# Optimization experiments

Measured on AMD Instinct MI355X. Metric: run time of the kernel, lower is better.

Reference implementation:

```python
import jax, jax.numpy as jnp
import numpy as np

E = 20000      # num edges
S = 64         # mul of 0e (scalar) channels
V = 32         # mul of 1o (vector) channels
FC_IN = 128    # radial basis length
HID = 64       # fc hidden width
INV_SQRT3 = 0.5773502691896258  # CG(1o x 1o -> 0e) = delta_ij / sqrt(3)


def setup_inputs() -> dict:
    key = jax.random.key(0)
    ks = jax.random.split(key, 16)
    n = jax.random.normal
    return {
        # edge features, layout [64 scalars | 32 vectors * 3 comps]
        "fea_in1": n(ks[0], (E, S + 3 * V), jnp.float32),
        "fea_in2": n(ks[1], (E, S + 3 * V), jnp.float32),
        "fea_weight": n(ks[2], (E, FC_IN), jnp.float32),
        # FullyConnectedTensorProduct internal weights (e3nn init: normal(0,1))
        "w_ss_s": n(ks[3], (S, S, S), jnp.float32),   # 0e x 0e -> 64x0e scalars
        "w_vv_s": n(ks[4], (V, V, S), jnp.float32),   # 1o x 1o -> 64x0e scalars
        "w_ss_g": n(ks[5], (S, S, V), jnp.float32),   # 0e x 0e -> 32x0e gates
        "w_vv_g": n(ks[6], (V, V, V), jnp.float32),   # 1o x 1o -> 32x0e gates
        "w_sv_v": n(ks[7], (S, V, V), jnp.float32),   # 0e x 1o -> 32x1o
        "w_vs_v": n(ks[8], (V, S, V), jnp.float32),   # 1o x 0e -> 32x1o
        # fc MLP: Linear(128,64) SiLU Linear(64,64) SiLU Linear(64,96)
        "fc_w1": n(ks[9], (FC_IN, HID), jnp.float32) / np.sqrt(FC_IN).astype(np.float32),
        "fc_b1": jnp.zeros((HID,), jnp.float32),
        "fc_w2": n(ks[10], (HID, HID), jnp.float32) / np.sqrt(HID).astype(np.float32),
        "fc_b2": jnp.zeros((HID,), jnp.float32),
        "fc_w3": n(ks[11], (HID, S + V), jnp.float32) / np.sqrt(HID).astype(np.float32),
        "fc_b3": jnp.zeros((S + V,), jnp.float32),
        "batch_edge": jnp.zeros((E,), jnp.int32),  # unused (norm='')
    }


def _equiconv(fea_in1, fea_in2, fea_weight,
              w_ss_s, w_vv_s, w_ss_g, w_vv_g, w_sv_v, w_vs_v,
              fc_w1, fc_b1, fc_w2, fc_b2, fc_w3, fc_b3):
    x1s, x1v = fea_in1[:, :S], fea_in1[:, S:].reshape(-1, V, 3)
    x2s, x2v = fea_in2[:, :S], fea_in2[:, S:].reshape(-1, V, 3)

    # path normalization: 1/sqrt(fan_in), fan_in = sum(mul1*mul2) over paths to output
    a_sc = 1.0 / np.sqrt(S * S + V * V).astype(np.float32)
    a_vec = 1.0 / np.sqrt(2 * S * V).astype(np.float32)

    # FullyConnectedTensorProduct (uvw connectivity)
    sc = a_sc * (jnp.einsum('eu,ev,uvw->ew', x1s, x2s, w_ss_s)
                 + INV_SQRT3 * jnp.einsum('eui,evi,uvw->ew', x1v, x2v, w_vv_s))
    g = a_sc * (jnp.einsum('eu,ev,uvw->ew', x1s, x2s, w_ss_g)
                + INV_SQRT3 * jnp.einsum('eui,evi,uvw->ew', x1v, x2v, w_vv_g))
    vec = a_vec * (jnp.einsum('eu,evi,uvw->ewi', x1s, x2v, w_sv_v)
                   + jnp.einsum('eui,ev,uvw->ewi', x1v, x2s, w_vs_v))

    # Gate: silu on scalars, sigmoid gates multiply the l>0 part
    sc = jax.nn.silu(sc)
    vec = vec * jax.nn.sigmoid(g)[:, :, None]

    # fc MLP producing per-channel elementwise conv weights
    h = jax.nn.silu(fea_weight @ fc_w1 + fc_b1)
    h = jax.nn.silu(h @ fc_w2 + fc_b2)
    w = h @ fc_w3 + fc_b3  # [E, S+V]

    # e3ElementWise: one scalar weight per channel (shared over m components)
    sc = sc * w[:, :S]
    vec = vec * w[:, S:, None]
    return jnp.concatenate([sc, vec.reshape(-1, 3 * V)], axis=-1)


def reference(fea_in1, fea_in2, fea_weight,
              w_ss_s, w_vv_s, w_ss_g, w_vv_g, w_sv_v, w_vs_v,
              fc_w1, fc_b1, fc_w2, fc_b2, fc_w3, fc_b3, batch_edge):
    del batch_edge  # only used by optional e3LayerNorm (norm='')
    return _equiconv(fea_in1, fea_in2, fea_weight,
                     w_ss_s, w_vv_s, w_ss_g, w_vv_g, w_sv_v, w_vs_v,
                     fc_w1, fc_b1, fc_w2, fc_b2, fc_w3, fc_b3)
```

## Files before the change

### kernel.cpp

```cpp
#include <hip/hip_runtime.h>


#define E_TOT 20000

typedef __attribute__((ext_vector_type(8))) short short8;
typedef __attribute__((ext_vector_type(4))) float f32x4;
typedef __attribute__((ext_vector_type(2))) __bf16 bf16x2;

#define FRAG_USH 512
#define HALF_USH 1536
#define CH_USH   3072
#define N_CH     52
#define NSLOT    5
#define STRIDE_W 159744
#define FC1_OFF  638976
#define FC2_OFF  647168
#define FC3_OFF  651264
#define WS_USH   657408

#define X1S_OFF  61440
#define X1V_OFF  65664
#define POOL_B   71936

__device__ __forceinline__ unsigned short f2b(float f){
  return __builtin_bit_cast(unsigned short, (__bf16)f);
}
__device__ __forceinline__ unsigned f2b2(float lo, float hi){
  bf16x2 t; t[0] = (__bf16)lo; t[1] = (__bf16)hi;
  return __builtin_bit_cast(unsigned, t);
}
__device__ __forceinline__ float b2f(unsigned short h){
  return __uint_as_float(((unsigned)h) << 16);
}
__device__ __forceinline__ f32x4 mfma16(short8 a, short8 b, f32x4 c){
  return __builtin_amdgcn_mfma_f32_16x16x32_bf16(a, b, c, 0, 0, 0);
}
union U8 { short8 v; unsigned u[4]; };
__device__ __forceinline__ float silu_f(float x){ return x/(1.f+__expf(-x)); }
__device__ __forceinline__ float sigm_f(float x){ return 1.f/(1.f+__expf(-x)); }

#define PACK8(a, s, x) \
  a.u[0]=f2b2((s)*(x)[0],(s)*(x)[1]); a.u[1]=f2b2((s)*(x)[2],(s)*(x)[3]); \
  a.u[2]=f2b2((s)*(x)[4],(s)*(x)[5]); a.u[3]=f2b2((s)*(x)[6],(s)*(x)[7]);

#define WV(code) { __builtin_amdgcn_s_waitcnt(code); __builtin_amdgcn_sched_barrier(0); }
#define WL3      { __builtin_amdgcn_s_waitcnt(0xC37F); __builtin_amdgcn_sched_barrier(0); }

__device__ __forceinline__ int fpos(int kl, int n16){
  return (kl>>3)*128 + n16*8 + (kl&7);
}

__global__ void prep_weights(const float* __restrict__ ss_s, const float* __restrict__ ss_g,
                             const float* __restrict__ vv_s, const float* __restrict__ vv_g,
                             const float* __restrict__ sv,   const float* __restrict__ vs,
                             const float* __restrict__ w1,   const float* __restrict__ w2,
                             const float* __restrict__ w3,   unsigned short* __restrict__ wsb)
{
  int g = blockIdx.x * 256 + threadIdx.x;
  if (g >= WS_USH/8) return;
  const int dest = g << 3;
  const float A_SC  = 0.013975424859373686f;
  const float A_VV  = (float)(0.013975424859373686 * 0.5773502691896258);
  const float A_VEC = 0.015625f;

  const float* src = nullptr;
  int stride = 0;
  float scale = 1.f;

  if (dest < FC1_OFF) {
    int wave = dest / STRIDE_W;
    int off  = dest - wave*STRIDE_W;
    int c    = off / CH_USH;
    int rem  = off - c*CH_USH;
    int t    = rem >> 9;
    int p    = rem & 511;
    int kl   = (p >> 7) << 3;
    int n16  = (p >> 3) & 15;
    if (c < 32) {
      int u = (wave<<4) + (c>>1);
      int v = ((c&1)<<5) + kl;
      if (t < 4) { src = ss_s + (u<<12)+(v<<6)+((t<<4)+n16);     stride = 64; }
      else       { src = ss_g + (u<<11)+(v<<5)+(((t-4)<<4)+n16); stride = 32; }
      scale = A_SC;
    } else if (c < 40) {
      int u = (wave<<3) + (c-32);
      int v = kl;
      if (t < 4) { src = vv_s + (u<<11)+(v<<6)+((t<<4)+n16);     stride = 64; }
      else       { src = vv_g + (u<<10)+(v<<5)+(((t-4)<<4)+n16); stride = 32; }
      scale = A_VV;
    } else if (c < 46) {
      int ul = (c-40)*3 + (t>>1);
      if (ul < 16) {
        int u = (wave<<4) + ul;
        src = sv + (u<<10)+(kl<<5)+(((t&1)<<4)+n16);
        stride = 32; scale = A_VEC;
      }
    } else {
      int cc = c - 46;
      int vh = cc/3, ch3 = cc - vh*3;
      int fseq = ch3*6 + t;
      if (fseq < 16) {
        int u = (wave<<3) + (fseq>>1);
        int v = (vh<<5) + kl;
        src = vs + (u<<11)+(v<<5)+(((fseq&1)<<4)+n16);
        stride = 32; scale = A_VEC;
      }
    }
  } else if (dest < FC2_OFF) {
    int off = dest - FC1_OFF;
    int fi = off >> 9, p = off & 511;
    int kl = (p>>7)<<3, n16 = (p>>3)&15;
    int k = ((fi>>2)<<5) + kl, n = ((fi&3)<<4) + n16;
    src = w1 + (k<<6) + n; stride = 64;
  } else if (dest < FC3_OFF) {
    int off = dest - FC2_OFF;
    int fi = off >> 9, p = off & 511;
    int kl = (p>>7)<<3, n16 = (p>>3)&15;
    int k = ((fi>>2)<<5) + kl, n = ((fi&3)<<4) + n16;
    src = w2 + (k<<6) + n; stride = 64;
  } else {
    int off = dest - FC3_OFF;
    int fi = off >> 9, p = off & 511;
    int kl = (p>>7)<<3, n16 = (p>>3)&15;
    int koff = fi/6, nhi = fi - koff*6;
    int k = (koff<<5) + kl, n = (nhi<<4) + n16;
    src = w3 + k*96 + n; stride = 96;
  }

  U8 a;
  if (src) {
    float v0 = scale * src[0*stride], v1 = scale * src[1*stride];
    float v2 = scale * src[2*stride], v3 = scale * src[3*stride];
    float v4 = scale * src[4*stride], v5 = scale * src[5*stride];
    float v6 = scale * src[6*stride], v7 = scale * src[7*stride];
    a.u[0] = f2b2(v0, v1); a.u[1] = f2b2(v2, v3);
    a.u[2] = f2b2(v4, v5); a.u[3] = f2b2(v6, v7);
  } else {
    a.u[0] = 0; a.u[1] = 0; a.u[2] = 0; a.u[3] = 0;
  }
  *(short8*)(wsb + dest) = a.v;
}

__global__ __launch_bounds__(256, 2)
void equiconv_main(const float* __restrict__ fea1,
                   const float* __restrict__ fea2,
                   const float* __restrict__ few,
                   const float* __restrict__ fb1,
                   const float* __restrict__ fb2,
                   const float* __restrict__ fb3,
                   const unsigned short* __restrict__ wsb,
                   float* __restrict__ out)
{
  __shared__ __align__(16) unsigned char pool[POOL_B];
  unsigned short* ring = (unsigned short*)pool;
  unsigned short* x1s_ = (unsigned short*)(pool + X1S_OFF);
  unsigned short* x1v_ = (unsigned short*)(pool + X1V_OFF);
  unsigned short* hb_  = (unsigned short*)(pool + X1S_OFF);
  float*          redf = (float*)pool;

  #define X1S(r, cc) x1s_[(r)*66 + (cc)]
  #define X1V(r, cc) x1v_[(r)*98 + (cc)]
  #define HB(w, r, cc) hb_[(((w)<<4) + (r))*72 + (cc)]

  const int tid  = threadIdx.x;
  const int lane = tid & 63, wv = tid >> 6;
  const int ln   = lane & 15, quad = lane >> 4, q8 = quad << 3;
  const int ebase = blockIdx.x << 5;

  for (int it = tid; it < 1280; it += 256){
    int row = it / 40, seg = it - row*40;
    float4 v1 = *(const float4*)(fea1 + (size_t)(ebase + row)*160 + seg*4);
    const float* p1 = (const float*)&v1;
    int c0 = seg*4;
    #pragma unroll
    for (int jj = 0; jj < 4; jj++){
      int col = c0 + jj;
      if (col < 64) X1S(row, col) = f2b(p1[jj]);
      else          X1V(row, col-64) = f2b(p1[jj]);
    }
  }
  __syncthreads();

  float xe[2][8], xo[2][8], y0[2][8], y1[2][8], y2[2][8];
  #pragma unroll
  for (int s = 0; s < 2; s++){
    const float* p = fea2 + (size_t)(ebase + s*16 + ln)*160;
    float4 a0 = *(const float4*)(p + q8);
    float4 a1 = *(const float4*)(p + q8 + 4);
    float4 b0 = *(const float4*)(p + 32 + q8);
    float4 b1 = *(const float4*)(p + 36 + q8);
    xe[s][0]=a0.x; xe[s][1]=a0.y; xe[s][2]=a0.z; xe[s][3]=a0.w;
    xe[s][4]=a1.x; xe[s][5]=a1.y; xe[s][6]=a1.z; xe[s][7]=a1.w;
    xo[s][0]=b0.x; xo[s][1]=b0.y; xo[s][2]=b0.z; xo[s][3]=b0.w;
    xo[s][4]=b1.x; xo[s][5]=b1.y; xo[s][6]=b1.z; xo[s][7]=b1.w;
    const float* py = p + 64 + q8*3;
    float yb[24];
    #pragma unroll
    for (int t = 0; t < 12; t++){
      float2 f2v = *(const float2*)(py + 2*t);
      yb[2*t] = f2v.x; yb[2*t+1] = f2v.y;
    }
    #pragma unroll
    for (int j = 0; j < 8; j++){
      y0[s][j] = yb[3*j]; y1[s][j] = yb[3*j+1]; y2[s][j] = yb[3*j+2];
    }
  }

  const unsigned short* gstream = wsb + (size_t)wv*STRIDE_W;
  const int rbase = wv*NSLOT*HALF_USH;
  auto issue_half = [&](int h){
    const unsigned short* g = gstream + h*HALF_USH + lane*8;
    unsigned short* l = &ring[rbase + (h%NSLOT)*HALF_USH];
    #pragma unroll
    for (int q = 0; q < 3; q++)
      __builtin_amdgcn_global_load_lds(
        (const __attribute__((address_space(1))) unsigned int*)(g + q*FRAG_USH),
        (__attribute__((address_space(3))) unsigned int*)(l + q*FRAG_USH),
        16, 0, 0);
  };
  issue_half(0); issue_half(1); issue_half(2); issue_half(3);

  const int r0 = ln, r1 = 16 + ln;
  const f32x4 z4 = {0.f,0.f,0.f,0.f};
  f32x4 accS[2][6] = {{z4,z4,z4,z4,z4,z4},{z4,z4,z4,z4,z4,z4}};
  f32x4 accV[2][3][2] = {{{z4,z4},{z4,z4},{z4,z4}},{{z4,z4},{z4,z4},{z4,z4}}};

  #define READCH(cc, bb, WAC, WBC, DOISS) { \
    const int h0_ = 2*(cc); \
    const int sA_ = h0_ % NSLOT, sB_ = (h0_+1) % NSLOT; \
    WV(WAC); \
    { const unsigned short* pA_ = &ring[rbase + sA_*HALF_USH + lane*8]; \
      bb[0] = *(const short8*)(pA_); \
      bb[1] = *(const short8*)(pA_ + FRAG_USH); \
      bb[2] = *(const short8*)(pA_ + 2*FRAG_USH); } \
    __builtin_amdgcn_sched_barrier(0); \
    if (DOISS) issue_half(h0_ + 4); \
    WV(WBC); \
    { const unsigned short* pB_ = &ring[rbase + sB_*HALF_USH + lane*8]; \
      bb[3] = *(const short8*)(pB_); \
      bb[4] = *(const short8*)(pB_ + FRAG_USH); \
      bb[5] = *(const short8*)(pB_ + 2*FRAG_USH); } \
    __builtin_amdgcn_sched_barrier(0); \
    if (DOISS) { WL3; issue_half(h0_ + 5); } }

  #pragma unroll 2
  for (int c = 0; c < 32; c++){
    int u = (wv<<4) + (c>>1);
    float s0 = b2f(X1S(r0, u));
    float s1 = b2f(X1S(r1, u));
    U8 a0, a1;
    if (c & 1){ PACK8(a0, s0, xo[0]); PACK8(a1, s1, xo[1]); }
    else      { PACK8(a0, s0, xe[0]); PACK8(a1, s1, xe[1]); }
    short8 bb[6];
    READCH(c, bb, 0x0F79, 0x0F79, 1);
    #pragma unroll
    for (int t = 0; t < 6; t++){
      accS[0][t] = mfma16(a0.v, bb[t], accS[0][t]);
      accS[1][t] = mfma16(a1.v, bb[t], accS[1][t]);
    }
  }
  #pragma unroll 1
  for (int k8 = 0; k8 < 8; k8++){
    int c = 32 + k8, u = (wv<<3) + k8;
    U8 a[2];
    #pragma unroll
    for (int s = 0; s < 2; s++){
      int rr = s ? r1 : r0;
      float c0 = b2f(X1V(rr, u*3+0));
      float c1 = b2f(X1V(rr, u*3+1));
      float c2 = b2f(X1V(rr, u*3+2));
      float pv[8];
      #pragma unroll
      for (int j = 0; j < 8; j++)
        pv[j] = c0*y0[s][j] + c1*y1[s][j] + c2*y2[s][j];
      a[s].u[0]=f2b2(pv[0],pv[1]); a[s].u[1]=f2b2(pv[2],pv[3]);
      a[s].u[2]=f2b2(pv[4],pv[5]); a[s].u[3]=f2b2(pv[6],pv[7]);
    }
    short8 bb[6];
    READCH(c, bb, 0x0F79, 0x0F79, 1);
    #pragma unroll
    for (int t = 0; t < 6; t++){
      accS[0][t] = mfma16(a[0].v, bb[t], accS[0][t]);
      accS[1][t] = mfma16(a[1].v, bb[t], accS[1][t]);
    }
  }
  #pragma unroll 1
  for (int ch = 0; ch < 6; ch++){
    int c = 40 + ch;
    short8 bb[6];
    READCH(c, bb, 0x0F79, 0x0F79, 1);
    #pragma unroll
    for (int uu = 0; uu < 3; uu++){
      int ui = ch*3 + uu;
      if (ui < 16){
        int u = (wv<<4) + ui;
        float s0 = b2f(X1S(r0, u));
        float s1 = b2f(X1S(r1, u));
        U8 a[2][3];
        PACK8(a[0][0], s0, y0[0]); PACK8(a[0][1], s0, y1[0]); PACK8(a[0][2], s0, y2[0]);
        PACK8(a[1][0], s1, y0[1]); PACK8(a[1][1], s1, y1[1]); PACK8(a[1][2], s1, y2[1]);
        #pragma unroll
        for (int t = 0; t < 2; t++){
          short8 b8 = bb[uu*2 + t];
          #pragma unroll
          for (int s = 0; s < 2; s++)
            #pragma unroll
            for (int i = 0; i < 3; i++)
              accV[s][i][t] = mfma16(a[s][i].v, b8, accV[s][i][t]);
        }
      }
    }
  }
  #define VSBODY(pcv, bb) { \
    const int p_ = (pcv)/3, ch_ = (pcv) - p_*3; \
    _Pragma("unroll") \
    for (int uu = 0; uu < 3; uu++){ \
      int ui = ch_*3 + uu; \
      if (ui < 8){ \
        int u = (wv<<3) + ui; \
        U8 a[2][3]; \
        _Pragma("unroll") \
        for (int s = 0; s < 2; s++){ \
          int rr = s ? r1 : r0; \
          float c0 = b2f(X1V(rr, u*3+0)); \
          float c1 = b2f(X1V(rr, u*3+1)); \
          float c2 = b2f(X1V(rr, u*3+2)); \
          const float* xx = p_ ? xo[s] : xe[s]; \
          PACK8(a[s][0], c0, xx); PACK8(a[s][1], c1, xx); PACK8(a[s][2], c2, xx); \
        } \
        _Pragma("unroll") \
        for (int t = 0; t < 2; t++){ \
          short8 b8 = bb[uu*2 + t]; \
          _Pragma("unroll") \
          for (int s = 0; s < 2; s++) \
            _Pragma("unroll") \
            for (int i = 0; i < 3; i++) \
              accV[s][i][t] = mfma16(a[s][i].v, b8, accV[s][i][t]); \
        } \
      } \
    } }

  #pragma unroll 1
  for (int pc = 0; pc < 4; pc++){
    short8 bb[6];
    READCH(46+pc, bb, 0x0F79, 0x0F79, 1);
    VSBODY(pc, bb);
  }
  {
    short8 bb[6];
    READCH(50, bb, 0x0F79, 0x0F76, 0);
    VSBODY(4, bb);
  }
  {
    short8 bb[6];
    READCH(51, bb, 0x0F73, 0x0F70, 0);
    VSBODY(5, bb);
  }

  f32x4 T0[12], T1[12];
  #pragma unroll
  for (int t = 0; t < 6; t++){ T0[t] = accS[0][t]; T1[t] = accS[1][t]; }
  #pragma unroll
  for (int t = 0; t < 2; t++)
    #pragma unroll
    for (int i = 0; i < 3; i++){
      T0[6+3*t+i] = accV[0][i][t]; T1[6+3*t+i] = accV[1][i][t];
    }

  #define PUT12(base, T) { _Pragma("unroll") for (int j=0;j<12;j++) \
    *(f32x4*)(redf + ((base)+j)*320 + ln*20 + (quad<<2)) = T[j]; }
  #define ADD12(base, T) { _Pragma("unroll") for (int j=0;j<12;j++) \
    T[j] += *(const f32x4*)(redf + ((base)+j)*320 + ln*20 + (quad<<2)); }

  __syncthreads();
  if (wv==1) PUT12(0, T0);  if (wv==2) PUT12(12, T1);
  __syncthreads();
  if (wv==0) ADD12(0, T0);  if (wv==3) ADD12(12, T1);
  __syncthreads();
  if (wv==2) PUT12(0, T0);  if (wv==1) PUT12(12, T1);
  __syncthreads();
  if (wv==0) ADD12(0, T0);  if (wv==3) ADD12(12, T1);
  __syncthreads();
  if (wv==3) PUT12(0, T0);  if (wv==0) PUT12(12, T1);
  __syncthreads();
  if (wv==0) ADD12(0, T0);  if (wv==3) ADD12(12, T1);

  if (wv == 1 || wv == 2) return;
  const int s = (wv == 0) ? 0 : 1;
  f32x4* P = (wv == 0) ? T0 : T1;

  f32x4 accF[4] = {z4,z4,z4,z4};
  {
    const float* fwp = few + (size_t)(ebase + s*16 + ln)*128;
    const short8* B = (const short8*)(wsb + FC1_OFF);
    #pragma unroll
    for (int c = 0; c < 4; c++){
      float4 fa  = *(const float4*)(fwp + c*32 + q8);
      float4 fbv = *(const float4*)(fwp + c*32 + q8 + 4);
      U8 a;
      a.u[0]=f2b2(fa.x,fa.y);   a.u[1]=f2b2(fa.z,fa.w);
      a.u[2]=f2b2(fbv.x,fbv.y); a.u[3]=f2b2(fbv.z,fbv.w);
      #pragma unroll
      for (int t = 0; t < 4; t++) accF[t] = mfma16(a.v, B[(c*4+t)*64 + lane], accF[t]);
    }
  }
  #pragma unroll
  for (int t = 0; t < 4; t++){
    float bb = fb1[(t<<4)+ln];
    #pragma unroll
    for (int r = 0; r < 4; r++)
      HB(wv, (quad<<2)+r, (t<<4)+ln) = f2b(silu_f(accF[t][r] + bb));
  }
  f32x4 acc2[4] = {z4,z4,z4,z4};
  {
    const short8* B = (const short8*)(wsb + FC2_OFF);
    #pragma unroll
    for (int c = 0; c < 2; c++){
      uint4 hq = *(const uint4*)&HB(wv, ln, c*32 + q8);
      U8 a; a.u[0]=hq.x; a.u[1]=hq.y; a.u[2]=hq.z; a.u[3]=hq.w;
      #pragma unroll
      for (int t = 0; t < 4; t++) acc2[t] = mfma16(a.v, B[(c*4+t)*64 + lane], acc2[t]);
    }
  }
  #pragma unroll
  for (int t = 0; t < 4; t++){
    float bb = fb2[(t<<4)+ln];
    #pragma unroll
    for (int r = 0; r < 4; r++)
      HB(wv, (quad<<2)+r, (t<<4)+ln) = f2b(silu_f(acc2[t][r] + bb));
  }
  f32x4 acc3[6] = {z4,z4,z4,z4,z4,z4};
  {
    const short8* B = (const short8*)(wsb + FC3_OFF);
    #pragma unroll
    for (int c = 0; c < 2; c++){
      uint4 hq = *(const uint4*)&HB(wv, ln, c*32 + q8);
      U8 a; a.u[0]=hq.x; a.u[1]=hq.y; a.u[2]=hq.z; a.u[3]=hq.w;
      #pragma unroll
      for (int t = 0; t < 6; t++) acc3[t] = mfma16(a.v, B[(c*6+t)*64 + lane], acc3[t]);
    }
  }

  #pragma unroll
  for (int r = 0; r < 4; r++){
    int eg = ebase + s*16 + (quad<<2) + r;
    float* op = out + (size_t)eg*160;
    #pragma unroll
    for (int t = 0; t < 4; t++)
      op[(t<<4)+ln] = silu_f(P[t][r]) * (acc3[t][r] + fb3[(t<<4)+ln]);
    #pragma unroll
    for (int tp = 0; tp < 2; tp++){
      int wc = (tp<<4) + ln;
      float f = sigm_f(P[4+tp][r]) * (acc3[4+tp][r] + fb3[64+wc]);
      op[64 + wc*3 + 0] = P[6+3*tp+0][r] * f;
      op[64 + wc*3 + 1] = P[6+3*tp+1][r] * f;
      op[64 + wc*3 + 2] = P[6+3*tp+2][r] * f;
    }
  }
}

extern "C" void kernel_launch(void* const* d_in, const int* in_sizes, int n_in,
                              void* d_out, int out_size, void* d_ws, size_t ws_size,
                              hipStream_t stream) {
  (void)in_sizes; (void)n_in; (void)out_size; (void)ws_size;
  unsigned short* wsb = (unsigned short*)d_ws;

  prep_weights<<<(WS_USH/8 + 255)/256, 256, 0, stream>>>(
      (const float*)d_in[3], (const float*)d_in[5],
      (const float*)d_in[4], (const float*)d_in[6],
      (const float*)d_in[7], (const float*)d_in[8],
      (const float*)d_in[9], (const float*)d_in[11], (const float*)d_in[13],
      wsb);

  equiconv_main<<<E_TOT/32, 256, 0, stream>>>(
      (const float*)d_in[0], (const float*)d_in[1], (const float*)d_in[2],
      (const float*)d_in[10], (const float*)d_in[12], (const float*)d_in[14],
      (const unsigned short*)wsb, (float*)d_out);
}
```

Before: 176.1 us.

## Shrink weight ring to 3 slots, pack fea2 registers as bf16, raise occupancy

After: 191.2 us. 8.6% more time.

```diff
diff --git a/kernel.cpp b/kernel.cpp
--- a/kernel.cpp
+++ b/kernel.cpp
@@ -11,16 +11,16 @@
 #define HALF_USH 1536
 #define CH_USH   3072
 #define N_CH     52
-#define NSLOT    5
+#define NSLOT    3
 #define STRIDE_W 159744
 #define FC1_OFF  638976
 #define FC2_OFF  647168
 #define FC3_OFF  651264
 #define WS_USH   657408
 
-#define X1S_OFF  61440
-#define X1V_OFF  65664
-#define POOL_B   71936
+#define X1S_OFF  36864
+#define X1V_OFF  41088
+#define POOL_B   47360
 
 __device__ __forceinline__ unsigned short f2b(float f){
   return __builtin_bit_cast(unsigned short, (__bf16)f);
@@ -32,6 +32,8 @@
 __device__ __forceinline__ float b2f(unsigned short h){
   return __uint_as_float(((unsigned)h) << 16);
 }
+__device__ __forceinline__ float ulo(unsigned u){ return __uint_as_float(u << 16); }
+__device__ __forceinline__ float uhi(unsigned u){ return __uint_as_float(u & 0xFFFF0000u); }
 __device__ __forceinline__ f32x4 mfma16(short8 a, short8 b, f32x4 c){
   return __builtin_amdgcn_mfma_f32_16x16x32_bf16(a, b, c, 0, 0, 0);
 }
@@ -39,12 +41,14 @@
 __device__ __forceinline__ float silu_f(float x){ return x/(1.f+__expf(-x)); }
 __device__ __forceinline__ float sigm_f(float x){ return 1.f/(1.f+__expf(-x)); }
 
-#define PACK8(a, s, x) \
-  a.u[0]=f2b2((s)*(x)[0],(s)*(x)[1]); a.u[1]=f2b2((s)*(x)[2],(s)*(x)[3]); \
-  a.u[2]=f2b2((s)*(x)[4],(s)*(x)[5]); a.u[3]=f2b2((s)*(x)[6],(s)*(x)[7]);
-
-#define WV(code) { __builtin_amdgcn_s_waitcnt(code); __builtin_amdgcn_sched_barrier(0); }
-#define WL3      { __builtin_amdgcn_s_waitcnt(0xC37F); __builtin_amdgcn_sched_barrier(0); }
+#define PACK8P(a, s, xp) { \
+  a.u[0]=f2b2((s)*ulo((xp)[0]),(s)*uhi((xp)[0])); \
+  a.u[1]=f2b2((s)*ulo((xp)[1]),(s)*uhi((xp)[1])); \
+  a.u[2]=f2b2((s)*ulo((xp)[2]),(s)*uhi((xp)[2])); \
+  a.u[3]=f2b2((s)*ulo((xp)[3]),(s)*uhi((xp)[3])); }
+
+#define WVC(code) { __builtin_amdgcn_s_waitcnt(code); __builtin_amdgcn_sched_barrier(0xF); }
+#define GUARD     { __builtin_amdgcn_s_waitcnt(0xC07F); __builtin_amdgcn_sched_barrier(0xF); }
 
 __device__ __forceinline__ int fpos(int kl, int n16){
   return (kl>>3)*128 + n16*8 + (kl&7);
@@ -141,7 +145,7 @@
   *(short8*)(wsb + dest) = a.v;
 }
 
-__global__ __launch_bounds__(256, 2)
+__global__ __launch_bounds__(256, 3)
 void equiconv_main(const float* __restrict__ fea1,
                    const float* __restrict__ fea2,
                    const float* __restrict__ few,
@@ -181,7 +185,7 @@
   }
   __syncthreads();
 
-  float xe[2][8], xo[2][8], y0[2][8], y1[2][8], y2[2][8];
+  unsigned xep[2][4], xop[2][4], y0p[2][4], y1p[2][4], y2p[2][4];
   #pragma unroll
   for (int s = 0; s < 2; s++){
     const float* p = fea2 + (size_t)(ebase + s*16 + ln)*160;
@@ -189,10 +193,10 @@
     float4 a1 = *(const float4*)(p + q8 + 4);
     float4 b0 = *(const float4*)(p + 32 + q8);
     float4 b1 = *(const float4*)(p + 36 + q8);
-    xe[s][0]=a0.x; xe[s][1]=a0.y; xe[s][2]=a0.z; xe[s][3]=a0.w;
-    xe[s][4]=a1.x; xe[s][5]=a1.y; xe[s][6]=a1.z; xe[s][7]=a1.w;
-    xo[s][0]=b0.x; xo[s][1]=b0.y; xo[s][2]=b0.z; xo[s][3]=b0.w;
-    xo[s][4]=b1.x; xo[s][5]=b1.y; xo[s][6]=b1.z; xo[s][7]=b1.w;
+    xep[s][0]=f2b2(a0.x,a0.y); xep[s][1]=f2b2(a0.z,a0.w);
+    xep[s][2]=f2b2(a1.x,a1.y); xep[s][3]=f2b2(a1.z,a1.w);
+    xop[s][0]=f2b2(b0.x,b0.y); xop[s][1]=f2b2(b0.z,b0.w);
+    xop[s][2]=f2b2(b1.x,b1.y); xop[s][3]=f2b2(b1.z,b1.w);
     const float* py = p + 64 + q8*3;
     float yb[24];
     #pragma unroll
@@ -201,8 +205,10 @@
       yb[2*t] = f2v.x; yb[2*t+1] = f2v.y;
     }
     #pragma unroll
-    for (int j = 0; j < 8; j++){
-      y0[s][j] = yb[3*j]; y1[s][j] = yb[3*j+1]; y2[s][j] = yb[3*j+2];
+    for (int q = 0; q < 4; q++){
+      y0p[s][q] = f2b2(yb[6*q+0], yb[6*q+3]);
+      y1p[s][q] = f2b2(yb[6*q+1], yb[6*q+4]);
+      y2p[s][q] = f2b2(yb[6*q+2], yb[6*q+5]);
     }
   }
 
@@ -218,30 +224,27 @@
         (__attribute__((address_space(3))) unsigned int*)(l + q*FRAG_USH),
         16, 0, 0);
   };
-  issue_half(0); issue_half(1); issue_half(2); issue_half(3);
+  issue_half(0); issue_half(1); issue_half(2);
 
   const int r0 = ln, r1 = 16 + ln;
   const f32x4 z4 = {0.f,0.f,0.f,0.f};
   f32x4 accS[2][6] = {{z4,z4,z4,z4,z4,z4},{z4,z4,z4,z4,z4,z4}};
   f32x4 accV[2][3][2] = {{{z4,z4},{z4,z4},{z4,z4}},{{z4,z4},{z4,z4},{z4,z4}}};
 
-  #define READCH(cc, bb, WAC, WBC, DOISS) { \
+  #define READCH(cc, bb, WA, IA, WB, IB) { \
     const int h0_ = 2*(cc); \
-    const int sA_ = h0_ % NSLOT, sB_ = (h0_+1) % NSLOT; \
-    WV(WAC); \
-    { const unsigned short* pA_ = &ring[rbase + sA_*HALF_USH + lane*8]; \
+    WVC(WA); \
+    { const unsigned short* pA_ = &ring[rbase + (h0_%NSLOT)*HALF_USH + lane*8]; \
       bb[0] = *(const short8*)(pA_); \
       bb[1] = *(const short8*)(pA_ + FRAG_USH); \
       bb[2] = *(const short8*)(pA_ + 2*FRAG_USH); } \
-    __builtin_amdgcn_sched_barrier(0); \
-    if (DOISS) issue_half(h0_ + 4); \
-    WV(WBC); \
-    { const unsigned short* pB_ = &ring[rbase + sB_*HALF_USH + lane*8]; \
+    if (IA) { GUARD; issue_half(h0_ + 3); } \
+    WVC(WB); \
+    { const unsigned short* pB_ = &ring[rbase + ((h0_+1)%NSLOT)*HALF_USH + lane*8]; \
       bb[3] = *(const short8*)(pB_); \
       bb[4] = *(const short8*)(pB_ + FRAG_USH); \
       bb[5] = *(const short8*)(pB_ + 2*FRAG_USH); } \
-    __builtin_amdgcn_sched_barrier(0); \
-    if (DOISS) { WL3; issue_half(h0_ + 5); } }
+    if (IB) { GUARD; issue_half(h0_ + 4); } }
 
   #pragma unroll 2
   for (int c = 0; c < 32; c++){
@@ -249,10 +252,10 @@
     float s0 = b2f(X1S(r0, u));
     float s1 = b2f(X1S(r1, u));
     U8 a0, a1;
-    if (c & 1){ PACK8(a0, s0, xo[0]); PACK8(a1, s1, xo[1]); }
-    else      { PACK8(a0, s0, xe[0]); PACK8(a1, s1, xe[1]); }
-    short8 bb[6];
-    READCH(c, bb, 0x0F79, 0x0F79, 1);
+    if (c & 1){ PACK8P(a0, s0, xop[0]); PACK8P(a1, s1, xop[1]); }
+    else      { PACK8P(a0, s0, xep[0]); PACK8P(a1, s1, xep[1]); }
+    short8 bb[6];
+    READCH(c, bb, 0x0F76, 1, 0x0F76, 1);
     #pragma unroll
     for (int t = 0; t < 6; t++){
       accS[0][t] = mfma16(a0.v, bb[t], accS[0][t]);
@@ -269,15 +272,15 @@
       float c0 = b2f(X1V(rr, u*3+0));
       float c1 = b2f(X1V(rr, u*3+1));
       float c2 = b2f(X1V(rr, u*3+2));
-      float pv[8];
       #pragma unroll
-      for (int j = 0; j < 8; j++)
-        pv[j] = c0*y0[s][j] + c1*y1[s][j] + c2*y2[s][j];
-      a[s].u[0]=f2b2(pv[0],pv[1]); a[s].u[1]=f2b2(pv[2],pv[3]);
-      a[s].u[2]=f2b2(pv[4],pv[5]); a[s].u[3]=f2b2(pv[6],pv[7]);
-    }
-    short8 bb[6];
-    READCH(c, bb, 0x0F79, 0x0F79, 1);
+      for (int q = 0; q < 4; q++){
+        float lo = c0*ulo(y0p[s][q]) + c1*ulo(y1p[s][q]) + c2*ulo(y2p[s][q]);
+        float hi = c0*uhi(y0p[s][q]) + c1*uhi(y1p[s][q]) + c2*uhi(y2p[s][q]);
+        a[s].u[q] = f2b2(lo, hi);
+      }
+    }
+    short8 bb[6];
+    READCH(c, bb, 0x0F76, 1, 0x0F76, 1);
     #pragma unroll
     for (int t = 0; t < 6; t++){
       accS[0][t] = mfma16(a[0].v, bb[t], accS[0][t]);
@@ -288,7 +291,7 @@
   for (int ch = 0; ch < 6; ch++){
     int c = 40 + ch;
     short8 bb[6];
-    READCH(c, bb, 0x0F79, 0x0F79, 1);
+    READCH(c, bb, 0x0F76, 1, 0x0F76, 1);
     #pragma unroll
     for (int uu = 0; uu < 3; uu++){
       int ui = ch*3 + uu;
@@ -297,8 +300,8 @@
         float s0 = b2f(X1S(r0, u));
         float s1 = b2f(X1S(r1, u));
         U8 a[2][3];
-        PACK8(a[0][0], s0, y0[0]); PACK8(a[0][1], s0, y1[0]); PACK8(a[0][2], s0, y2[0]);
-        PACK8(a[1][0], s1, y0[1]); PACK8(a[1][1], s1, y1[1]); PACK8(a[1][2], s1, y2[1]);
+        PACK8P(a[0][0], s0, y0p[0]); PACK8P(a[0][1], s0, y1p[0]); PACK8P(a[0][2], s0, y2p[0]);
+        PACK8P(a[1][0], s1, y0p[1]); PACK8P(a[1][1], s1, y1p[1]); PACK8P(a[1][2], s1, y2p[1]);
         #pragma unroll
         for (int t = 0; t < 2; t++){
           short8 b8 = bb[uu*2 + t];
@@ -325,8 +328,8 @@
           float c0 = b2f(X1V(rr, u*3+0)); \
           float c1 = b2f(X1V(rr, u*3+1)); \
           float c2 = b2f(X1V(rr, u*3+2)); \
-          const float* xx = p_ ? xo[s] : xe[s]; \
-          PACK8(a[s][0], c0, xx); PACK8(a[s][1], c1, xx); PACK8(a[s][2], c2, xx); \
+          const unsigned* xx = p_ ? xop[s] : xep[s]; \
+          PACK8P(a[s][0], c0, xx); PACK8P(a[s][1], c1, xx); PACK8P(a[s][2], c2, xx); \
         } \
         _Pragma("unroll") \
         for (int t = 0; t < 2; t++){ \
@@ -343,17 +346,17 @@
   #pragma unroll 1
   for (int pc = 0; pc < 4; pc++){
     short8 bb[6];
-    READCH(46+pc, bb, 0x0F79, 0x0F79, 1);
+    READCH(46+pc, bb, 0x0F76, 1, 0x0F76, 1);
     VSBODY(pc, bb);
   }
   {
     short8 bb[6];
-    READCH(50, bb, 0x0F79, 0x0F76, 0);
+    READCH(50, bb, 0x0F76, 1, 0x0F76, 0);
     VSBODY(4, bb);
   }
   {
     short8 bb[6];
-    READCH(51, bb, 0x0F73, 0x0F70, 0);
+    READCH(51, bb, 0x0F73, 0, 0x0F70, 0);
     VSBODY(5, bb);
   }
 
```
